# Performance work log

Measured on AMD Instinct MI355X. Metric: run time of the kernel, lower is better.

The kernel has to match this reference:

```python
import jax, jax.numpy as jnp
import numpy as np

B, T, DMODEL = 2, 2048, 1024
H, DK, DV = 16, 64, 64
FF = 4096
EPS = 1e-5


def _layernorm_2d(x):
    # torch LayerNorm(normalized_shape=(T, dmodel)): normalize jointly over last two
    # dims, biased variance, weight=1 / bias=0 (freshly constructed each forward).
    mu = jnp.mean(x, axis=(1, 2), keepdims=True)
    var = jnp.mean((x - mu) ** 2, axis=(1, 2), keepdims=True)
    return (x - mu) / jnp.sqrt(var + EPS)


def setup_inputs() -> dict:
    key = jax.random.key(0)
    ks = jax.random.split(key, 9)
    s = 0.02  # small init for numerical sanity (original uses uniform(-1,1))
    return {
        "x": jax.random.normal(ks[0], (B, T, DMODEL), jnp.float32),
        "Wq": jax.random.normal(ks[1], (H, DMODEL, DK), jnp.float32) * s,
        "Wk": jax.random.normal(ks[2], (H, DMODEL, DK), jnp.float32) * s,
        "Wv": jax.random.normal(ks[3], (H, DMODEL, DV), jnp.float32) * s,
        "Wo": jax.random.normal(ks[4], (DMODEL, DMODEL), jnp.float32) * s,
        "W1": jax.random.normal(ks[5], (DMODEL, FF), jnp.float32) * s,
        "b1": jnp.zeros((FF,), jnp.float32),
        "W2": jax.random.normal(ks[6], (FF, DMODEL), jnp.float32) * s,
        "b2": jnp.zeros((DMODEL,), jnp.float32),
    }


def reference(x, Wq, Wk, Wv, Wo, W1, b1, W2, b2):
    b, t, d = x.shape
    h, _, dk = Wq.shape
    dv = Wv.shape[-1]
    # per-head projections: (B,H,T,dk/dv)
    Qp = jnp.einsum("btd,hdk->bhtk", x, Wq)
    Kp = jnp.einsum("btd,hdk->bhtk", x, Wk)
    Vp = jnp.einsum("btd,hdv->bhtv", x, Wv)
    scores = jnp.einsum("bhqk,bhsk->bhqs", Qp, Kp) / np.sqrt(dk).astype(np.float32)
    # NOTE: original does torch.softmax(heads, 2) -> softmax over the QUERY axis
    attn = jax.nn.softmax(scores, axis=2)
    heads = jnp.einsum("bhqs,bhsv->bqhv", attn, Vp).reshape(b, t, h * dv)
    att_out = heads @ Wo
    o1 = _layernorm_2d(x + att_out)
    ff = jnp.maximum(o1 @ W1 + b1, 0.0) @ W2 + b2
    return _layernorm_2d(o1 + ff)
```

## Files before the change

### kernel.cpp

```cpp
#include <hip/hip_runtime.h>
#include <hip/hip_bf16.h>
#include <cstddef>
#include <cstdint>

typedef __hip_bfloat16 hbf;
typedef __attribute__((ext_vector_type(8))) __bf16 bf16x8;
typedef __attribute__((ext_vector_type(4))) float f32x4;

#define B_ 2
#define T_ 2048
#define D_ 1024
#define H_ 16
#define FF_ 4096
#define EPS_ 1e-5f
#define SCALE_ 0.18033688011112f

__device__ __forceinline__ float bf2f(hbf v) { return __bfloat162float(v); }
__device__ __forceinline__ float fexp2(float x) {
  return __builtin_amdgcn_exp2f(x);
}
__device__ __forceinline__ float flog2(float x) {
  return __builtin_amdgcn_logf(x);
}
__device__ __forceinline__ float ldin(const void* p, size_t i, int isbf) {
  return isbf ? __bfloat162float(((const hbf*)p)[i]) : ((const float*)p)[i];
}
__device__ __forceinline__ void ston(void* p, size_t i, float v, int isbf) {
  if (isbf) ((hbf*)p)[i] = __float2bfloat16(v);
  else ((float*)p)[i] = v;
}
__device__ __forceinline__ f32x4 mfma16(bf16x8 a, bf16x8 b, f32x4 c) {
  return __builtin_amdgcn_mfma_f32_16x16x32_bf16(a, b, c, 0, 0, 0);
}
__device__ __forceinline__ bf16x8 ldfrag(const hbf* p) {
  return *(const bf16x8*)p;
}
__device__ __forceinline__ void glds16(const hbf* g, hbf* l) {
  __builtin_amdgcn_global_load_lds(
      (const __attribute__((address_space(1))) void*)g,
      (__attribute__((address_space(3))) void*)l, 16, 0, 0);
}

__global__ __launch_bounds__(256) void detect_dtype(const unsigned* x,
                                                    int* flag) {
  __shared__ int cnt[256];
  int c = 0;
  for (int i = threadIdx.x; i < 4096; i += 256) {
    unsigned low = x[i] & 0xFFFFu;
    unsigned e = (low >> 7) & 0xFFu;
    if (e >= 100u && e <= 142u) c++;
  }
  cnt[threadIdx.x] = c;
  __syncthreads();
  for (int off = 128; off > 0; off >>= 1) {
    if ((int)threadIdx.x < off) cnt[threadIdx.x] += cnt[threadIdx.x + off];
    __syncthreads();
  }
  if (threadIdx.x == 0) *flag = (cnt[0] > 2458) ? 1 : 0;
}

__device__ __forceinline__ void tr_tile(const void* __restrict__ src,
                                        hbf* __restrict__ dst, int R, int C,
                                        size_t zoff, int cx, int ry, int f,
                                        float (*tile)[33]) {
  const int tx = threadIdx.x & 31, ty = threadIdx.x >> 5;
  const int c0 = cx * 32, r0 = ry * 32;
#pragma unroll
  for (int p = 0; p < 4; p++) {
    int rr = p * 8 + ty;
    tile[rr][tx] = ldin(src, zoff + (size_t)(r0 + rr) * C + c0 + tx, f);
  }
  __syncthreads();
#pragma unroll
  for (int p = 0; p < 4; p++) {
    int cc = p * 8 + ty;
    dst[zoff + (size_t)(c0 + cc) * R + r0 + tx] = __float2bfloat16(tile[tx][cc]);
  }
}

__global__ __launch_bounds__(256) void preconv(
    const void* __restrict__ x, const void* __restrict__ Wq,
    const void* __restrict__ Wk, const void* __restrict__ Wv,
    const void* __restrict__ Wo, const void* __restrict__ W1,
    const void* __restrict__ W2, const void* __restrict__ b1,
    const void* __restrict__ b2, hbf* __restrict__ xb,
    hbf* __restrict__ wqkvt, hbf* __restrict__ wot, hbf* __restrict__ w1t,
    hbf* __restrict__ w2t, hbf* __restrict__ b1b, hbf* __restrict__ b2b,
    const int* __restrict__ flag) {
  __shared__ float tile[32][33];
  const int f = *flag;
  const int bid = blockIdx.x;
  if (bid < 3072) {
    int which = bid >> 10;
    int r = bid & 1023;
    int z = r >> 6, rem = r & 63;
    int ry = rem >> 1, cx = rem & 1;
    const void* src = (which == 0) ? Wq : (which == 1) ? Wk : Wv;
    hbf* dst = wqkvt + (size_t)which * (D_ * D_);
    tr_tile(src, dst, 1024, 64, (size_t)z * 65536, cx, ry, f, tile);
  } else if (bid < 4096) {
    int t = bid - 3072;
    tr_tile(Wo, wot, 1024, 1024, 0, t & 31, t >> 5, f, tile);
  } else if (bid < 8192) {
    int t = bid - 4096;
    tr_tile(W1, w1t, 1024, 4096, 0, t & 127, t >> 7, f, tile);
  } else if (bid < 12288) {
    int t = bid - 8192;
    tr_tile(W2, w2t, 4096, 1024, 0, t & 31, t >> 5, f, tile);
  } else if (bid < 13312) {
    size_t base = (size_t)(bid - 12288) * 4096;
    if (f) {
      const uint4* src = (const uint4*)((const hbf*)x + base);
      uint4* dst = (uint4*)(xb + base);
      for (int i = threadIdx.x; i < 512; i += 256) dst[i] = src[i];
    } else {
      const float4* src = (const float4*)((const float*)x + base);
      for (int i = threadIdx.x; i < 512; i += 256) {
        float4 a = src[i * 2], b = src[i * 2 + 1];
        union {
          hbf h[8];
          uint4 u;
        } o;
        o.h[0] = __float2bfloat16(a.x);
        o.h[1] = __float2bfloat16(a.y);
        o.h[2] = __float2bfloat16(a.z);
        o.h[3] = __float2bfloat16(a.w);
        o.h[4] = __float2bfloat16(b.x);
        o.h[5] = __float2bfloat16(b.y);
        o.h[6] = __float2bfloat16(b.z);
        o.h[7] = __float2bfloat16(b.w);
        *(uint4*)(xb + base + (size_t)i * 8) = o.u;
      }
    }
  } else if (bid == 13312) {
    for (int i = threadIdx.x; i < FF_; i += 256)
      b1b[i] = __float2bfloat16(ldin(b1, i, f));
  } else {
    for (int i = threadIdx.x; i < D_; i += 256)
      b2b[i] = __float2bfloat16(ldin(b2, i, f));
  }
}

template <int MODE, int BM, int BN, int BK>
__global__ __launch_bounds__(256) void gemm_bt(
    const hbf* __restrict__ A, const hbf* __restrict__ Bt, hbf* __restrict__ C,
    float* __restrict__ Cf0, float* __restrict__ Cf1,
    const hbf* __restrict__ e1, float* __restrict__ red, int M, int N, int K,
    int LDK) {
  constexpr int WM = BM / 2, WN = BN / 2;
  constexpr int IF = WM / 16, JF = WN / 16;
  constexpr int HK = BK / 32;
  constexpr int LPT = BK / 8;
  constexpr int CPR = 2048 / BK;
  __shared__ alignas(16) hbf As[BM * BK];
  __shared__ alignas(16) hbf Bs[BN * BK];
  const int tid = threadIdx.x;
  const int wave = tid >> 6, lane = tid & 63;
  const int quad = lane >> 4, l16 = lane & 15;
  const int m0 = blockIdx.y * BM, n0 = blockIdx.x * BN;
  const int mw = (wave >> 1) * WM, nw = (wave & 1) * WN;
  const int srow = tid / LPT;
  const int scol = (tid % LPT) * 8;
  const f32x4 zero = {0.f, 0.f, 0.f, 0.f};
  f32x4 acc[IF][JF];
#pragma unroll
  for (int i = 0; i < IF; i++)
#pragma unroll
    for (int j = 0; j < JF; j++) acc[i][j] = zero;

  const hbf* ga = &A[(size_t)(m0 + srow) * LDK + scol];
  const hbf* gb = &Bt[(size_t)(n0 + srow) * LDK + scol];
  hbf* lA = &As[wave * 512];
  hbf* lB = &Bs[wave * 512];

  for (int k0 = 0; k0 < K; k0 += BK) {
#pragma unroll
    for (int c = 0; c < BM / CPR; c++)
      glds16(ga + (size_t)(c * CPR) * LDK + k0, lA + c * 2048);
#pragma unroll
    for (int c = 0; c < BN / CPR; c++)
      glds16(gb + (size_t)(c * CPR) * LDK + k0, lB + c * 2048);
    __syncthreads();
    bf16x8 af[HK][IF], bfr[HK][JF];
#pragma unroll
    for (int h = 0; h < HK; h++) {
#pragma unroll
      for (int i = 0; i < IF; i++)
        af[h][i] = ldfrag(&As[(mw + i * 16 + l16) * BK + h * 32 + quad * 8]);
#pragma unroll
      for (int j = 0; j < JF; j++)
        bfr[h][j] = ldfrag(&Bs[(nw + j * 16 + l16) * BK + h * 32 + quad * 8]);
    }
#pragma unroll
    for (int h = 0; h < HK; h++)
#pragma unroll
      for (int i = 0; i < IF; i++)
#pragma unroll
        for (int j = 0; j < JF; j++)
          acc[i][j] = mfma16(af[h][i], bfr[h][j], acc[i][j]);
    __syncthreads();
  }
  float ssum = 0.f, ssq = 0.f;
#pragma unroll
  for (int i = 0; i < IF; i++)
#pragma unroll
    for (int j = 0; j < JF; j++)
#pragma unroll
      for (int r = 0; r < 4; r++) {
        int m = m0 + mw + i * 16 + quad * 4 + r;
        int n = n0 + nw + j * 16 + l16;
        float v = acc[i][j][r];
        if (MODE == 0) {
          int which = n >> 10, n1 = n & 1023;
          int h = n1 >> 6, cc = n1 & 63;
          int b = m >> 11, t = m & (T_ - 1);
          if (which == 0) v *= SCALE_;
          C[(size_t)which * ((size_t)B_ * H_ * T_ * 64) +
            (((size_t)(b * H_ + h)) * T_ + t) * 64 + cc] = __float2bfloat16(v);
        } else if (MODE == 1) {
          hbf hv = __float2bfloat16(v + bf2f(e1[(size_t)m * N + n]));
          C[(size_t)m * N + n] = hv;
          float fv = bf2f(hv);
          ssum += fv;
          ssq += fv * fv;
        } else if (MODE == 2) {
          C[(size_t)m * N + n] = __float2bfloat16(fmaxf(v + bf2f(e1[n]), 0.f));
        } else if (MODE == 5) {
          const hbf* bias = (const hbf*)Cf0;
          hbf hv = __float2bfloat16(v + bf2f(bias[n]) +
                                    bf2f(e1[(size_t)m * N + n]));
          C[(size_t)m * N + n] = hv;
          float fv = bf2f(hv);
          ssum += fv;
          ssq += fv * fv;
        }
      }
  if (MODE == 1 || MODE == 5) {
    float* sc = (float*)As;
    sc[tid] = ssum;
    sc[256 + tid] = ssq;
    __syncthreads();
    for (int off = 128; off > 0; off >>= 1) {
      if (tid < off) {
        sc[tid] += sc[tid + off];
        sc[256 + tid] += sc[256 + tid + off];
      }
      __syncthreads();
    }
    if (tid == 0) {
      int b = m0 >> 11;
      atomicAdd(&red[b * 2 + 0], sc[0]);
      atomicAdd(&red[b * 2 + 1], sc[256]);
    }
  }
}

__global__ __launch_bounds__(256) void attn_stats(const hbf* __restrict__ Q,
                                                  const hbf* __restrict__ K,
                                                  const hbf* __restrict__ V,
                                                  hbf* __restrict__ Vt) {
  __shared__ alignas(16) hbf Ks[64 * 72];
  __shared__ alignas(16) hbf Qs[64 * 72];
  __shared__ float sAdj[64];
  const int bh = blockIdx.y;
  const int s0 = blockIdx.x * 64;
  const int tid = threadIdx.x;
  const int wave = tid >> 6, lane = tid & 63;
  const int quad = lane >> 4, l16 = lane & 15;
  const int sw = wave * 16;
  const hbf* Kb = K + (size_t)bh * T_ * 64;
  const hbf* Qb = Q + (size_t)bh * T_ * 64;
  const hbf* Vb = V + (size_t)bh * T_ * 64;
  hbf* Vtb = Vt + (size_t)bh * 64 * T_;
  const int r_ = tid >> 3, c_ = (tid & 7) * 8;
#pragma unroll
  for (int c = 0; c < 2; c++) {
    int row = c * 32 + r_;
    *(float4*)(&Ks[row * 72 + c_]) =
        *(const float4*)(&Kb[(size_t)(s0 + row) * 64 + c_]);
  }
  __syncthreads();
  bf16x8 kf0 = ldfrag(&Ks[(sw + l16) * 72 + quad * 8]);
  bf16x8 kf1 = ldfrag(&Ks[(sw + l16) * 72 + 32 + quad * 8]);
  float m_thr[4], l_thr[4];
#pragma unroll
  for (int r = 0; r < 4; r++) {
    m_thr[r] = -1e30f;
    l_thr[r] = 0.f;
  }
  const f32x4 zero = {0.f, 0.f, 0.f, 0.f};
  for (int qt = 0; qt < T_ / 64; qt++) {
    if (qt) __syncthreads();
#pragma unroll
    for (int c = 0; c < 2; c++) {
      int row = c * 32 + r_;
      *(float4*)(&Qs[row * 72 + c_]) =
          *(const float4*)(&Qb[(size_t)(qt * 64 + row) * 64 + c_]);
    }
    __syncthreads();
    f32x4 acc[4];
#pragma unroll
    for (int j = 0; j < 4; j++) {
      bf16x8 qf0 = ldfrag(&Qs[(j * 16 + l16) * 72 + quad * 8]);
      bf16x8 qf1 = ldfrag(&Qs[(j * 16 + l16) * 72 + 32 + quad * 8]);
      f32x4 a = zero;
      a = mfma16(kf0, qf0, a);
      a = mfma16(kf1, qf1, a);
      acc[j] = a;
    }
#pragma unroll
    for (int r = 0; r < 4; r++) {
      float mt = fmaxf(fmaxf(acc[0][r], acc[1][r]),
                       fmaxf(acc[2][r], acc[3][r]));
      float nm = fmaxf(m_thr[r], mt);
      float s = l_thr[r] * fexp2(m_thr[r] - nm);
#pragma unroll
      for (int j = 0; j < 4; j++) s += fexp2(acc[j][r] - nm);
      l_thr[r] = s;
      m_thr[r] = nm;
    }
  }
#pragma unroll
  for (int d = 1; d < 16; d <<= 1) {
#pragma unroll
    for (int r = 0; r < 4; r++) {
      float om = __shfl_xor(m_thr[r], d);
      float ol = __shfl_xor(l_thr[r], d);
      float nm = fmaxf(m_thr[r], om);
      l_thr[r] = l_thr[r] * fexp2(m_thr[r] - nm) + ol * fexp2(om - nm);
      m_thr[r] = nm;
    }
  }
  if (l16 == 0) {
#pragma unroll
    for (int r = 0; r < 4; r++)
      sAdj[sw + quad * 4 + r] = m_thr[r] + flog2(l_thr[r]);
  }
  __syncthreads();
#pragma unroll
  for (int c = 0; c < 2; c++) {
    int e = (c * 256 + tid) * 8;
    int r = e >> 6, col = e & 63;
    union alignas(16) {
      hbf h[8];
      float4 f4;
    } u;
    u.f4 = *(const float4*)(&Vb[(size_t)(s0 + r) * 64 + col]);
    float sc = fexp2(-sAdj[r]);
#pragma unroll
    for (int k2 = 0; k2 < 8; k2++)
      u.h[k2] = __float2bfloat16(bf2f(u.h[k2]) * sc);
    *(float4*)(&Ks[r * 72 + col]) = u.f4;
  }
  __syncthreads();
#pragma unroll
  for (int c = 0; c < 2; c++) {
    int e = (c * 256 + tid) * 8;
    int v = e >> 6, tt = e & 63;
    union alignas(16) {
      hbf h[8];
      float4 f4;
    } u;
#pragma unroll
    for (int k2 = 0; k2 < 8; k2++) u.h[k2] = Ks[(tt + k2) * 72 + v];
    *(float4*)(&Vtb[(size_t)v * T_ + s0 + tt]) = u.f4;
  }
}

__global__ __launch_bounds__(256) void attn_apply(const hbf* __restrict__ Q,
                                                  const hbf* __restrict__ K,
                                                  const hbf* __restrict__ Vt,
                                                  hbf* __restrict__ heads) {
  __shared__ alignas(16) hbf Ksb[2 * 64 * 64];
  __shared__ alignas(16) hbf Vsb[3 * 64 * 64];
  __shared__ alignas(16) hbf Ps[4 * 2 * 32 * 72];
  const int bh = blockIdx.y;
  const int b = bh >> 4, h = bh & 15;
  const int q0 = blockIdx.x * 128;
  const int tid = threadIdx.x;
  const int wave = tid >> 6, lane = tid & 63;
  const int quad = lane >> 4, l16 = lane & 15;
  const int qw = wave * 32;
  const hbf* Qb = Q + (size_t)bh * T_ * 64;
  const hbf* Kb = K + (size_t)bh * T_ * 64;
  const hbf* Vtb = Vt + (size_t)bh * 64 * T_;
  hbf* Pw = &Ps[wave * (2 * 32 * 72)];
  const int srow = tid >> 3, sc8 = tid & 7;
  const int swz = sc8 ^ (srow & 7);
  const hbf* gk = Kb + (size_t)srow * 64 + swz * 8;
  const hbf* gv = Vtb + (size_t)srow * T_ + swz * 8;
  hbf* lK = &Ksb[wave * 512];
  hbf* lV = &Vsb[wave * 512];
  const int sx = (l16 & 7) * 8;
  bf16x8 qf[2][2];
#pragma unroll
  for (int i = 0; i < 2; i++)
#pragma unroll
    for (int hh = 0; hh < 2; hh++)
      qf[i][hh] = ldfrag(&Qb[(size_t)(q0 + qw + i * 16 + l16) * 64 + hh * 32 +
                             quad * 8]);
  const f32x4 zero = {0.f, 0.f, 0.f, 0.f};
  f32x4 accO[2][4];
#pragma unroll
  for (int i = 0; i < 2; i++)
#pragma unroll
    for (int j = 0; j < 4; j++) accO[i][j] = zero;

  glds16(gk, lK);
  glds16(gk + 2048, lK + 2048);
  glds16(gv, lV);
  glds16(gv + (size_t)32 * T_, lV + 2048);
  glds16(gk + 4096, lK + 4096);
  glds16(gk + 4096 + 2048, lK + 4096 + 2048);
  glds16(gv + 64, lV + 4096);
  glds16(gv + (size_t)32 * T_ + 64, lV + 4096 + 2048);
  __syncthreads();

  {
    const hbf* Kc = &Ksb[0];
    bf16x8 kf[4][2];
#pragma unroll
    for (int j = 0; j < 4; j++)
#pragma unroll
      for (int hh = 0; hh < 2; hh++)
        kf[j][hh] =
            ldfrag(&Kc[(j * 16 + l16) * 64 + ((hh * 32 + quad * 8) ^ sx)]);
    __builtin_amdgcn_s_setprio(1);
    f32x4 accS[2][4];
#pragma unroll
    for (int i = 0; i < 2; i++)
#pragma unroll
      for (int j = 0; j < 4; j++) {
        f32x4 a = mfma16(kf[j][0], qf[i][0], zero);
        accS[i][j] = mfma16(kf[j][1], qf[i][1], a);
      }
    __builtin_amdgcn_s_setprio(0);
#pragma unroll
    for (int i = 0; i < 2; i++)
#pragma unroll
      for (int j = 0; j < 4; j++) {
        union {
          hbf h4[4];
          uint2 u;
        } pk;
#pragma unroll
        for (int r = 0; r < 4; r++)
          pk.h4[r] = __float2bfloat16(fexp2(accS[i][j][r]));
        *(uint2*)&Pw[(i * 16 + l16) * 72 + j * 16 + quad * 4] = pk.u;
      }
  }
  __syncthreads();

  for (int st = 1; st < T_ / 64; st++) {
    const int kcur = st & 1;
    const int pcur = st & 1, pprev = pcur ^ 1;
    const int vprev = (st - 1) % 3;
    if (st < T_ / 64 - 1) {
      const int knxt = (st + 1) & 1, vnxt = (st + 1) % 3;
      size_t ko = (size_t)(st + 1) * 4096;
      glds16(gk + ko, lK + knxt * 4096);
      glds16(gk + ko + 2048, lK + knxt * 4096 + 2048);
      glds16(gv + (st + 1) * 64, lV + vnxt * 4096);
      glds16(gv + (size_t)32 * T_ + (st + 1) * 64, lV + vnxt * 4096 + 2048);
    }
    const hbf* Kc = &Ksb[kcur * 4096];
    const hbf* Vp = &Vsb[vprev * 4096];
    bf16x8 kf[4][2];
#pragma unroll
    for (int j = 0; j < 4; j++)
#pragma unroll
      for (int hh = 0; hh < 2; hh++)
        kf[j][hh] =
            ldfrag(&Kc[(j * 16 + l16) * 64 + ((hh * 32 + quad * 8) ^ sx)]);
    bf16x8 pf[2][2];
#pragma unroll
    for (int i = 0; i < 2; i++)
#pragma unroll
      for (int hh = 0; hh < 2; hh++)
        pf[i][hh] = ldfrag(
            &Pw[pprev * (32 * 72) + (i * 16 + l16) * 72 + hh * 32 + quad * 8]);
    __builtin_amdgcn_s_setprio(1);
#pragma unroll
    for (int j2 = 0; j2 < 4; j2++) {
      bf16x8 vf0 = ldfrag(&Vp[(j2 * 16 + l16) * 64 + ((quad * 8) ^ sx)]);
      bf16x8 vf1 = ldfrag(&Vp[(j2 * 16 + l16) * 64 + ((32 + quad * 8) ^ sx)]);
#pragma unroll
      for (int i = 0; i < 2; i++) {
        accO[i][j2] = mfma16(pf[i][0], vf0, accO[i][j2]);
        accO[i][j2] = mfma16(pf[i][1], vf1, accO[i][j2]);
      }
    }
    f32x4 accS[2][4];
#pragma unroll
    for (int i = 0; i < 2; i++)
#pragma unroll
      for (int j = 0; j < 4; j++) {
        f32x4 a = mfma16(kf[j][0], qf[i][0], zero);
        accS[i][j] = mfma16(kf[j][1], qf[i][1], a);
      }
    __builtin_amdgcn_s_setprio(0);
#pragma unroll
    for (int i = 0; i < 2; i++)
#pragma unroll
      for (int j = 0; j < 4; j++) {
        union {
          hbf h4[4];
          uint2 u;
        } pk;
#pragma unroll
        for (int r = 0; r < 4; r++)
          pk.h4[r] = __float2bfloat16(fexp2(accS[i][j][r]));
        *(uint2*)&Pw[pcur * (32 * 72) + (i * 16 + l16) * 72 + j * 16 +
                     quad * 4] = pk.u;
      }
    __syncthreads();
  }
  {
    const int pl = (T_ / 64 - 1) & 1;
    const hbf* Vp = &Vsb[((T_ / 64 - 1) % 3) * 4096];
    bf16x8 pf[2][2];
#pragma unroll
    for (int i = 0; i < 2; i++)
#pragma unroll
      for (int hh = 0; hh < 2; hh++)
        pf[i][hh] = ldfrag(
            &Pw[pl * (32 * 72) + (i * 16 + l16) * 72 + hh * 32 + quad * 8]);
    __builtin_amdgcn_s_setprio(1);
#pragma unroll
    for (int j2 = 0; j2 < 4; j2++) {
      bf16x8 vf0 = ldfrag(&Vp[(j2 * 16 + l16) * 64 + ((quad * 8) ^ sx)]);
      bf16x8 vf1 = ldfrag(&Vp[(j2 * 16 + l16) * 64 + ((32 + quad * 8) ^ sx)]);
#pragma unroll
      for (int i = 0; i < 2; i++) {
        accO[i][j2] = mfma16(pf[i][0], vf0, accO[i][j2]);
        accO[i][j2] = mfma16(pf[i][1], vf1, accO[i][j2]);
      }
    }
    __builtin_amdgcn_s_setprio(0);
  }
#pragma unroll
  for (int i = 0; i < 2; i++)
#pragma unroll
    for (int j2 = 0; j2 < 4; j2++)
#pragma unroll
      for (int r = 0; r < 4; r++) {
        int q = q0 + qw + i * 16 + quad * 4 + r;
        int v = j2 * 16 + l16;
        heads[((size_t)(b * T_ + q)) * D_ + h * 64 + v] =
            __float2bfloat16(accO[i][j2][r]);
      }
}

__global__ __launch_bounds__(256) void ln_norm(const hbf* __restrict__ src,
                                               const float* __restrict__ red,
                                               void* dst,
                                               const int* __restrict__ flag,
                                               int force_bf) {
  const int isbf = force_bf ? 1 : *flag;
  const float invN = 1.f / (float)(T_ * D_);
  for (size_t i = (size_t)blockIdx.x * 256 + threadIdx.x;
       i < (size_t)B_ * T_ * D_; i += (size_t)gridDim.x * 256) {
    int b = (int)(i >> 21);
    float mu = red[b * 2 + 0] * invN;
    float var = red[b * 2 + 1] * invN - mu * mu;
    ston(dst, i, (bf2f(src[i]) - mu) * rsqrtf(var + EPS_), isbf);
  }
}

__global__ __launch_bounds__(256) void ln2_norm(const hbf* __restrict__ r2,
                                                const float* __restrict__ red,
                                                void* dst,
                                                const int* __restrict__ flag) {
  const int isbf = *flag;
  const float invN = 1.f / (float)(T_ * D_);
  const uint2* r2v = (const uint2*)r2;
  for (size_t i = (size_t)blockIdx.x * 256 + threadIdx.x;
       i < (size_t)B_ * T_ * D_ / 4; i += (size_t)gridDim.x * 256) {
    int b = (int)(i >> 19);
    float mu = red[b * 2 + 0] * invN;
    float var = red[b * 2 + 1] * invN - mu * mu;
    float rstd = rsqrtf(var + EPS_);
    union {
      uint2 u;
      hbf h[4];
    } s;
    s.u = r2v[i];
    float out[4];
#pragma unroll
    for (int r = 0; r < 4; r++) out[r] = (bf2f(s.h[r]) - mu) * rstd;
    if (isbf) {
      union {
        hbf h[4];
        uint2 u;
      } pk;
#pragma unroll
      for (int r = 0; r < 4; r++) pk.h[r] = __float2bfloat16(out[r]);
      ((uint2*)dst)[i] = pk.u;
    } else {
      float4 f{out[0], out[1], out[2], out[3]};
      ((float4*)dst)[i] = f;
    }
  }
}

extern "C" void kernel_launch(void* const* d_in, const int* in_sizes, int n_in,
                              void* d_out, int out_size, void* d_ws,
                              size_t ws_size, hipStream_t stream) {
  const void* x = d_in[0];
  const void* Wq = d_in[1];
  const void* Wk = d_in[2];
  const void* Wv = d_in[3];
  const void* Wo = d_in[4];
  const void* W1 = d_in[5];
  const void* W2 = d_in[7];
  const void* b1 = d_in[6];
  const void* b2 = d_in[8];

  const size_t MB = 1024 * 1024;
  if (ws_size < 89 * MB) return;

  char* w = (char*)d_ws;
  hbf* xb = (hbf*)(w + 0 * MB);
  hbf* wqkvt = (hbf*)(w + 8 * MB);
  hbf* wot = (hbf*)(w + 14 * MB);
  hbf* w1t = (hbf*)(w + 16 * MB);
  hbf* w2t = (hbf*)(w + 24 * MB);
  hbf* Qb = (hbf*)(w + 32 * MB);
  hbf* Kb = (hbf*)(w + 40 * MB);
  hbf* Vb = (hbf*)(w + 48 * MB);
  hbf* Vtb = (hbf*)(w + 56 * MB);
  hbf* heads = (hbf*)(w + 64 * MB);
  hbf* r1 = (hbf*)(w + 72 * MB);
  hbf* o1 = (hbf*)(w + 80 * MB);
  hbf* ff1 = (hbf*)(w + 32 * MB);
  hbf* r2 = (hbf*)(w + 0 * MB);
  hbf* b1b = (hbf*)(w + 88 * MB);
  hbf* b2b = b1b + FF_;
  float* red = (float*)(b2b + D_);
  int* flag = (int*)(red + 8);

  hipMemsetAsync(red, 0, 8 * sizeof(float) + sizeof(int), stream);
  detect_dtype<<<1, 256, 0, stream>>>((const unsigned*)x, flag);

  const int M = B_ * T_;
  preconv<<<13314, 256, 0, stream>>>(x, Wq, Wk, Wv, Wo, W1, W2, b1, b2, xb,
                                     wqkvt, wot, w1t, w2t, b1b, b2b, flag);
  gemm_bt<0, 128, 128, 64><<<dim3(24, 32), 256, 0, stream>>>(
      xb, wqkvt, Qb, nullptr, nullptr, nullptr, nullptr, M, 3 * D_, D_, D_);
  attn_stats<<<dim3(32, 32), 256, 0, stream>>>(Qb, Kb, Vb, Vtb);
  attn_apply<<<dim3(16, 32), 256, 0, stream>>>(Qb, Kb, Vtb, heads);
  gemm_bt<1, 128, 64, 128><<<dim3(16, 32), 256, 0, stream>>>(
      heads, wot, r1, nullptr, nullptr, xb, red, M, D_, D_, D_);
  ln_norm<<<4096, 256, 0, stream>>>(r1, red, o1, flag, 1);
  gemm_bt<2, 128, 128, 64><<<dim3(32, 32), 256, 0, stream>>>(
      o1, w1t, ff1, nullptr, nullptr, b1b, nullptr, M, FF_, D_, D_);
  gemm_bt<5, 128, 64, 128><<<dim3(16, 32), 256, 0, stream>>>(
      ff1, w2t, r2, (float*)b2b, nullptr, o1, red + 4, M, D_, FF_, FF_);
  ln2_norm<<<2048, 256, 0, stream>>>(r2, red + 4, d_out, flag);
}
```

Before: 481.8 us.

## Split-K the FF2 GEMM into two fp32 partials and fuse residual into LN2

The second feed-forward GEMM (K=4096) now runs as a split-K launch with two K halves on grid z, each writing fp32 partial results, and uses 128x128 tiles instead of 128x64. The bias, residual add and LayerNorm statistics move into a new ln2_stats kernel, and ln2_norm recomputes the sum from the partials. This is meant to give the long-K GEMM more parallel blocks and a shorter per-block loop. The cost is an extra kernel and roughly 32MB of fp32 partial traffic that is read twice. The out-projection GEMM tile BK also changes from 128 to 64.

```diff
diff --git a/kernel.cpp b/kernel.cpp
--- a/kernel.cpp
+++ b/kernel.cpp
@@ -161,6 +161,7 @@
   const int mw = (wave >> 1) * WM, nw = (wave & 1) * WN;
   const int srow = tid / LPT;
   const int scol = (tid % LPT) * 8;
+  const int kbase = (MODE == 4) ? blockIdx.z * K : 0;
   const f32x4 zero = {0.f, 0.f, 0.f, 0.f};
   f32x4 acc[IF][JF];
 #pragma unroll
@@ -168,8 +169,8 @@
 #pragma unroll
     for (int j = 0; j < JF; j++) acc[i][j] = zero;
 
-  const hbf* ga = &A[(size_t)(m0 + srow) * LDK + scol];
-  const hbf* gb = &Bt[(size_t)(n0 + srow) * LDK + scol];
+  const hbf* ga = &A[(size_t)(m0 + srow) * LDK + kbase + scol];
+  const hbf* gb = &Bt[(size_t)(n0 + srow) * LDK + kbase + scol];
   hbf* lA = &As[wave * 512];
   hbf* lB = &Bs[wave * 512];
 
@@ -225,17 +226,12 @@
           ssq += fv * fv;
         } else if (MODE == 2) {
           C[(size_t)m * N + n] = __float2bfloat16(fmaxf(v + bf2f(e1[n]), 0.f));
-        } else if (MODE == 5) {
-          const hbf* bias = (const hbf*)Cf0;
-          hbf hv = __float2bfloat16(v + bf2f(bias[n]) +
-                                    bf2f(e1[(size_t)m * N + n]));
-          C[(size_t)m * N + n] = hv;
-          float fv = bf2f(hv);
-          ssum += fv;
-          ssq += fv * fv;
+        } else if (MODE == 4) {
+          float* Cf = blockIdx.z ? Cf1 : Cf0;
+          Cf[(size_t)m * N + n] = v;
         }
       }
-  if (MODE == 1 || MODE == 5) {
+  if (MODE == 1) {
     float* sc = (float*)As;
     sc[tid] = ssum;
     sc[256 + tid] = ssq;
@@ -567,27 +563,79 @@
   }
 }
 
-__global__ __launch_bounds__(256) void ln2_norm(const hbf* __restrict__ r2,
-                                                const float* __restrict__ red,
-                                                void* dst,
-                                                const int* __restrict__ flag) {
+__global__ __launch_bounds__(256) void ln2_stats(const float* __restrict__ P0,
+                                                 const float* __restrict__ P1,
+                                                 const hbf* __restrict__ o1,
+                                                 const hbf* __restrict__ b2b,
+                                                 float* __restrict__ red) {
+  __shared__ float s1[256], s2[256];
+  const int b = blockIdx.y;
+  const size_t base = (size_t)b * (T_ * D_ / 4);
+  const float4* P0v = (const float4*)P0;
+  const float4* P1v = (const float4*)P1;
+  const uint2* o1v = (const uint2*)o1;
+  const uint2* b2v = (const uint2*)b2b;
+  float sum = 0.f, sq = 0.f;
+  for (size_t i = (size_t)blockIdx.x * 256 + threadIdx.x;
+       i < (size_t)(T_ * D_ / 4); i += (size_t)gridDim.x * 256) {
+    float4 p0 = P0v[base + i], p1 = P1v[base + i];
+    union {
+      uint2 u;
+      hbf h[4];
+    } o, bb;
+    o.u = o1v[base + i];
+    bb.u = b2v[i & (D_ / 4 - 1)];
+#pragma unroll
+    for (int r = 0; r < 4; r++) {
+      float v = (&p0.x)[r] + (&p1.x)[r] + bf2f(bb.h[r]) + bf2f(o.h[r]);
+      sum += v;
+      sq += v * v;
+    }
+  }
+  s1[threadIdx.x] = sum;
+  s2[threadIdx.x] = sq;
+  __syncthreads();
+  for (int off = 128; off > 0; off >>= 1) {
+    if ((int)threadIdx.x < off) {
+      s1[threadIdx.x] += s1[threadIdx.x + off];
+      s2[threadIdx.x] += s2[threadIdx.x + off];
+    }
+    __syncthreads();
+  }
+  if (threadIdx.x == 0) {
+    atomicAdd(&red[b * 2 + 0], s1[0]);
+    atomicAdd(&red[b * 2 + 1], s2[0]);
+  }
+}
+
+__global__ __launch_bounds__(256) void ln2_norm(
+    const float* __restrict__ P0, const float* __restrict__ P1,
+    const hbf* __restrict__ o1, const hbf* __restrict__ b2b,
+    const float* __restrict__ red, void* dst, const int* __restrict__ flag) {
   const int isbf = *flag;
   const float invN = 1.f / (float)(T_ * D_);
-  const uint2* r2v = (const uint2*)r2;
+  const float4* P0v = (const float4*)P0;
+  const float4* P1v = (const float4*)P1;
+  const uint2* o1v = (const uint2*)o1;
+  const uint2* b2v = (const uint2*)b2b;
   for (size_t i = (size_t)blockIdx.x * 256 + threadIdx.x;
        i < (size_t)B_ * T_ * D_ / 4; i += (size_t)gridDim.x * 256) {
     int b = (int)(i >> 19);
     float mu = red[b * 2 + 0] * invN;
     float var = red[b * 2 + 1] * invN - mu * mu;
     float rstd = rsqrtf(var + EPS_);
+    float4 p0 = P0v[i], p1 = P1v[i];
     union {
       uint2 u;
       hbf h[4];
-    } s;
-    s.u = r2v[i];
+    } o, bb;
+    o.u = o1v[i];
+    bb.u = b2v[i & (D_ / 4 - 1)];
     float out[4];
 #pragma unroll
-    for (int r = 0; r < 4; r++) out[r] = (bf2f(s.h[r]) - mu) * rstd;
+    for (int r = 0; r < 4; r++)
+      out[r] =
+          ((&p0.x)[r] + (&p1.x)[r] + bf2f(bb.h[r]) + bf2f(o.h[r]) - mu) * rstd;
     if (isbf) {
       union {
         hbf h[4];
@@ -633,7 +681,8 @@
   hbf* r1 = (hbf*)(w + 72 * MB);
   hbf* o1 = (hbf*)(w + 80 * MB);
   hbf* ff1 = (hbf*)(w + 32 * MB);
-  hbf* r2 = (hbf*)(w + 0 * MB);
+  float* P0 = (float*)(w + 0 * MB);
+  float* P1 = (float*)(w + 64 * MB);
   hbf* b1b = (hbf*)(w + 88 * MB);
   hbf* b2b = b1b + FF_;
   float* red = (float*)(b2b + D_);
@@ -649,12 +698,13 @@
       xb, wqkvt, Qb, nullptr, nullptr, nullptr, nullptr, M, 3 * D_, D_, D_);
   attn_stats<<<dim3(32, 32), 256, 0, stream>>>(Qb, Kb, Vb, Vtb);
   attn_apply<<<dim3(16, 32), 256, 0, stream>>>(Qb, Kb, Vtb, heads);
-  gemm_bt<1, 128, 64, 128><<<dim3(16, 32), 256, 0, stream>>>(
+  gemm_bt<1, 128, 64, 64><<<dim3(16, 32), 256, 0, stream>>>(
       heads, wot, r1, nullptr, nullptr, xb, red, M, D_, D_, D_);
   ln_norm<<<4096, 256, 0, stream>>>(r1, red, o1, flag, 1);
   gemm_bt<2, 128, 128, 64><<<dim3(32, 32), 256, 0, stream>>>(
       o1, w1t, ff1, nullptr, nullptr, b1b, nullptr, M, FF_, D_, D_);
-  gemm_bt<5, 128, 64, 128><<<dim3(16, 32), 256, 0, stream>>>(
-      ff1, w2t, r2, (float*)b2b, nullptr, o1, red + 4, M, D_, FF_, FF_);
-  ln2_norm<<<2048, 256, 0, stream>>>(r2, red + 4, d_out, flag);
-}
+  gemm_bt<4, 128, 128, 64><<<dim3(8, 32, 2), 256, 0, stream>>>(
+      ff1, w2t, nullptr, P0, P1, nullptr, nullptr, M, D_, FF_ / 2, FF_);
+  ln2_stats<<<dim3(256, B_), 256, 0, stream>>>(P0, P1, o1, b2b, red + 4);
+  ln2_norm<<<2048, 256, 0, stream>>>(P0, P1, o1, b2b, red + 4, d_out, flag);
+}
```

After: 450.9 us. -6.4%, faster.
